# Performance work log

Hardware: AMD Instinct MI355X
Metric: run time of the kernel (lower is better)

## Reference

```python
import jax, jax.numpy as jnp
import numpy as np

N_ENT = 200000  # entities per graph (sr and tg)
E = 4_000_000   # triples per graph
R_SR, R_TG, D = 1000, 1200, 128


def _cosine_sim_nbyn(a, b):
    a = a * jax.lax.rsqrt(jnp.sum(a * a, -1, keepdims=True) + 1e-8)
    b = b * jax.lax.rsqrt(jnp.sum(b * b, -1, keepdims=True) + 1e-8)
    return a @ b.T


def _relation_weighting(a, b):
    # pad to square, cosine similarity, max-pool rows/cols (MuGNN RelationWeighting)
    ra, rb = a.shape[0], b.shape[0]
    n = max(ra, rb)
    a_p = jnp.pad(a, ((0, n - ra), (0, 0)))
    b_p = jnp.pad(b, ((0, n - rb), (0, 0)))
    sim = _cosine_sim_nbyn(a_p, b_p)  # [n, n]
    return jnp.max(sim, axis=1)[:ra], jnp.max(sim, axis=0)[:rb]


def _normalize_adj(rows, cols, vals, n):
    # symmetric normalization D^-1/2 A D^-1/2 on COO values
    deg = jax.ops.segment_sum(vals, rows, num_segments=n)
    d_is = jnp.where(deg > 0, jax.lax.rsqrt(jnp.maximum(deg, 1e-12)), 0.0)
    return vals * d_is[rows] * d_is[cols]


def _adjacency_side(head, tail, conf, imp, pca, n):
    # g_func_template: elementwise product of the three aligned sparse matrices
    vals = conf * imp * pca
    # + unit (identity) matrix, then normalize; coords = [edges ; diagonal]
    diag = jnp.arange(n)
    rows = jnp.concatenate([head, diag])
    cols = jnp.concatenate([tail, diag])
    allv = jnp.concatenate([vals, jnp.ones((n,), vals.dtype)])
    return _normalize_adj(rows, cols, allv, n)  # [E+n] COO values


def setup_inputs() -> dict:
    key = jax.random.key(0)
    ks = jax.random.split(key, 14)
    return {
        "rel_emb_sr": jax.random.normal(ks[0], (R_SR, D), jnp.float32),
        "rel_emb_tg": jax.random.normal(ks[1], (R_TG, D), jnp.float32),
        "conf_sr": jax.random.uniform(ks[2], (E,), jnp.float32),
        "imp_sr": jax.random.uniform(ks[3], (E,), jnp.float32),
        "pca_sr": jax.random.uniform(ks[4], (E,), jnp.float32),
        "conf_tg": jax.random.uniform(ks[5], (E,), jnp.float32),
        "imp_tg": jax.random.uniform(ks[6], (E,), jnp.float32),
        "pca_tg": jax.random.uniform(ks[7], (E,), jnp.float32),
        "head_sr": jax.random.randint(ks[8], (E,), 0, N_ENT),
        "tail_sr": jax.random.randint(ks[9], (E,), 0, N_ENT),
        "relation_sr": jax.random.randint(ks[10], (E,), 0, R_SR),
        "head_tg": jax.random.randint(ks[11], (E,), 0, N_ENT),
        "tail_tg": jax.random.randint(ks[12], (E,), 0, N_ENT),
        "relation_tg": jax.random.randint(ks[13], (E,), 0, R_TG),
    }


def reference(rel_emb_sr, rel_emb_tg, conf_sr, imp_sr, pca_sr,
              conf_tg, imp_tg, pca_tg,
              head_sr, tail_sr, relation_sr, head_tg, tail_tg, relation_tg):
    # relation weighting (computed in the original forward; g_func_template
    # discards the gathered relation attention, so relation_sr/tg do not
    # affect the adjacency values)
    rw_sr, rw_tg = _relation_weighting(rel_emb_sr, rel_emb_tg)
    adj_sr = _adjacency_side(head_sr, tail_sr, conf_sr, imp_sr, pca_sr, N_ENT)
    adj_tg = _adjacency_side(head_tg, tail_tg, conf_tg, imp_tg, pca_tg, N_ENT)
    # adjacency returned as normalized COO values on constant coords
    return adj_sr, adj_tg, rw_sr, rw_tg
```

## Files before the change

kernel.cpp:

```cpp
#include <hip/hip_runtime.h>
#include <stdint.h>

#define N_ENT 200000
#define NEDGE 4000000
#define RSR 1000
#define RTG 1200
#define DIM 128

#define NBUCK 196
#define BUCKSZ 1024
#define CAP 22272
#define CHUNK 4096
#define NE4 (NEDGE / 4)
#define NBLK 977
#define PER (NEDGE + N_ENT)
#define PER4 (PER / 4)
#define ATILES 16
#define BTILES 19
#define NRW 2240

typedef float f32x4 __attribute__((ext_vector_type(4)));
typedef int   i32x4 __attribute__((ext_vector_type(4)));


__global__ void prep_kernel(const float* __restrict__ emb_sr, const float* __restrict__ emb_tg,
                            float* __restrict__ an, float* __restrict__ bn,
                            unsigned* __restrict__ gcount) {
    int blk = blockIdx.x, t = threadIdx.x;
    const float* src; float* dst; int row;
    if (blk < RSR) { src = emb_sr; dst = an; row = blk; }
    else           { src = emb_tg; dst = bn; row = blk - RSR; }
    float x = src[row * DIM + t];
    __shared__ float sh[DIM];
    sh[t] = x * x;
    __syncthreads();
    for (int off = 64; off > 0; off >>= 1) {
        if (t < off) sh[t] += sh[t + off];
        __syncthreads();
    }
    dst[row * DIM + t] = x * rsqrtf(sh[0] + 1e-8f);
    if (blk == 0)
        for (int i = t; i < 2 * NBUCK; i += DIM) gcount[i] = 0;
}


__global__ __launch_bounds__(256) void passA_kernel(
        const float* __restrict__ conf_sr, const float* __restrict__ imp_sr,
        const float* __restrict__ pca_sr,
        const float* __restrict__ conf_tg, const float* __restrict__ imp_tg,
        const float* __restrict__ pca_tg,
        const int* __restrict__ head_sr, const int* __restrict__ head_tg,
        float* __restrict__ out_sr, float* __restrict__ out_tg,
        unsigned* __restrict__ gcount, unsigned* __restrict__ regions) {
    __shared__ unsigned cnt[NBUCK];
    __shared__ unsigned offs[NBUCK];
    __shared__ unsigned gdst[NBUCK];
    __shared__ unsigned ssum[256];
    __shared__ unsigned wtot[4];
    __shared__ unsigned stage[CHUNK];

    const int t = threadIdx.x;
    const int side = (int)blockIdx.x >= NBLK;
    const int blk = side ? blockIdx.x - NBLK : blockIdx.x;
    const f32x4* conf4 = (const f32x4*)(side ? conf_tg : conf_sr);
    const f32x4* imp4  = (const f32x4*)(side ? imp_tg  : imp_sr);
    const f32x4* pca4  = (const f32x4*)(side ? pca_tg  : pca_sr);
    const i32x4* head4 = (const i32x4*)(side ? head_tg : head_sr);
    f32x4*       o4    = (f32x4*)(side ? out_tg : out_sr);

    for (int i = t; i < NBUCK; i += 256) cnt[i] = 0;
    __syncthreads();

    int bkt[16];
    unsigned rec[16], rnk[16];
#pragma unroll
    for (int i = 0; i < 4; i++) {
        int q = blk * 1024 + t + i * 256;
        if (q < NE4) {
            f32x4 cf = __builtin_nontemporal_load(conf4 + q);
            f32x4 im = __builtin_nontemporal_load(imp4 + q);
            f32x4 pc = __builtin_nontemporal_load(pca4 + q);
            i32x4 hh = __builtin_nontemporal_load(head4 + q);
            f32x4 v = cf * im * pc;
            __builtin_nontemporal_store(v, o4 + q);
            const int hs[4] = {hh.x, hh.y, hh.z, hh.w};
            const float vs[4] = {v.x, v.y, v.z, v.w};
#pragma unroll
            for (int j = 0; j < 4; j++) {
                int h = hs[j];
                int bb = h >> 10;
                unsigned qv = (unsigned)(vs[j] * 16384.f + 0.5f);
                if (qv > 16383u) qv = 16383u;
                bkt[i * 4 + j] = bb;
                rec[i * 4 + j] = ((unsigned)h << 14) | qv;
                rnk[i * 4 + j] = atomicAdd(&cnt[bb], 1u);
            }
        } else {
#pragma unroll
            for (int j = 0; j < 4; j++) bkt[i * 4 + j] = -1;
        }
    }
    __syncthreads();

    {
        int lane = t & 63, w = t >> 6;
        unsigned s = (t < NBUCK) ? cnt[t] : 0u;
#pragma unroll
        for (int d = 1; d < 64; d <<= 1) {
            unsigned u = __shfl_up(s, d);
            if (lane >= d) s += u;
        }
        if (lane == 63) wtot[w] = s;
        ssum[t] = s;
    }
    __syncthreads();
    unsigned wb0 = wtot[0];
    unsigned wb1 = wb0 + wtot[1];
    unsigned wb2 = wb1 + wtot[2];
    unsigned total = wb2 + wtot[3];
    if (t < NBUCK) {
        int w = t >> 6;
        unsigned add = (w == 0) ? 0u : (w == 1) ? wb0 : (w == 2) ? wb1 : wb2;
        unsigned ex = ssum[t] + add - cnt[t];
        offs[t] = ex;
        unsigned gb = atomicAdd(&gcount[side * NBUCK + t], cnt[t]);
        gdst[t] = (unsigned)(side * NBUCK + t) * CAP + gb - ex;
    }
    __syncthreads();

#pragma unroll
    for (int i = 0; i < 16; i++)
        if (bkt[i] >= 0) stage[offs[bkt[i]] + rnk[i]] = rec[i];
    __syncthreads();

    for (int i = t; i < (int)total; i += 256) {
        unsigned r = stage[i];
        unsigned b = r >> 24;
        unsigned d = gdst[b] + i;
        if (d < (unsigned)(side * NBUCK + b + 1) * CAP)
            __builtin_nontemporal_store(r, regions + d);
    }
}


__global__ __launch_bounds__(256) void passB_kernel(const unsigned* __restrict__ regions,
                                                    const unsigned* __restrict__ gcount,
                                                    float* __restrict__ dis) {
    __shared__ float bins[BUCKSZ / 2];
    int t = threadIdx.x;
    int g = blockIdx.x;
    int sb = g >> 1;
    unsigned half = g & 1;
    for (int i = t; i < BUCKSZ / 2; i += 256) bins[i] = 0.f;
    __syncthreads();
    unsigned n = gcount[sb];
    if (n > CAP) n = CAP;
    const unsigned* rp = regions + (size_t)sb * CAP;
    for (unsigned i = t; i < n; i += 256) {
        unsigned r = __builtin_nontemporal_load(rp + i);
        unsigned bin = (r >> 14) & (BUCKSZ - 1);
        if ((bin >> 9) == half)
            atomicAdd(&bins[bin & 511u], (float)(r & 16383u) * (1.f / 16384.f));
    }
    __syncthreads();
    int side = sb >= NBUCK;
    int b = side ? sb - NBUCK : sb;
    int base = b * BUCKSZ + (int)half * 512;
    float* dout = dis + (size_t)side * N_ENT;
    for (int i = t; i < 512; i += 256) {
        int e = base + i;
        if (e < N_ENT) dout[e] = rsqrtf(1.0f + bins[i]);
    }
}


__global__ void deg_init_kernel(float* __restrict__ dis) {
    int i = blockIdx.x * 256 + threadIdx.x;
    if (i < (2 * N_ENT) / 4)
        ((float4*)dis)[i] = make_float4(1.f, 1.f, 1.f, 1.f);
}

__global__ void scatter_atomic_kernel(
        const float* __restrict__ conf_sr, const float* __restrict__ imp_sr,
        const float* __restrict__ pca_sr,
        const float* __restrict__ conf_tg, const float* __restrict__ imp_tg,
        const float* __restrict__ pca_tg,
        const int* __restrict__ head_sr, const int* __restrict__ head_tg,
        float* __restrict__ out_sr, float* __restrict__ out_tg,
        float* __restrict__ deg) {
    int e = blockIdx.x * blockDim.x + threadIdx.x;
    if (e < NEDGE) {
        float v = conf_sr[e] * imp_sr[e] * pca_sr[e];
        out_sr[e] = v;
        unsafeAtomicAdd(&deg[head_sr[e]], v);
    } else if (e < 2 * NEDGE) {
        int i = e - NEDGE;
        float v = conf_tg[i] * imp_tg[i] * pca_tg[i];
        out_tg[i] = v;
        unsafeAtomicAdd(&deg[N_ENT + head_tg[i]], v);
    }
}

__global__ void rsqrt_kernel(float* __restrict__ dis) {
    int i = blockIdx.x * blockDim.x + threadIdx.x;
    if (i < 2 * N_ENT) dis[i] = rsqrtf(dis[i]);
}


__global__ __launch_bounds__(256) void finalize_kernel(
        const int* __restrict__ head_sr, const int* __restrict__ tail_sr,
        const int* __restrict__ head_tg, const int* __restrict__ tail_tg,
        const float* __restrict__ dis, float* __restrict__ out,
        const float* __restrict__ rowpart, const float* __restrict__ colpart,
        float* __restrict__ rw_sr, float* __restrict__ rw_tg) {
    int idx = blockIdx.x * blockDim.x + threadIdx.x;
    if (idx >= 2 * PER4) {
        int rid = idx - 2 * PER4;
        if (rid < 1024) {
            if (rid < RSR) {
                float m = -1e30f;
                for (int b = 0; b < BTILES; b++) m = fmaxf(m, rowpart[b * 1024 + rid]);
                rw_sr[rid] = m;
            }
        } else if (rid < NRW) {
            int j = rid - 1024;
            if (j < RTG) {
                float m = -1e30f;
                for (int a = 0; a < ATILES; a++) m = fmaxf(m, colpart[a * 1216 + j]);
                rw_tg[j] = fmaxf(m, 0.0f);
            }
        }
        return;
    }
    int side = idx >= PER4 ? 1 : 0;
    int q = side ? idx - PER4 : idx;
    const float* dg = dis + (size_t)side * N_ENT;
    f32x4* o = (f32x4*)(out + (size_t)side * PER);
    if (q < NE4) {
        const i32x4* hd = (const i32x4*)(side ? head_tg : head_sr);
        const i32x4* tl = (const i32x4*)(side ? tail_tg : tail_sr);
        i32x4 hh = __builtin_nontemporal_load(hd + q);
        i32x4 tt = __builtin_nontemporal_load(tl + q);
        f32x4 v = __builtin_nontemporal_load(o + q);
        v.x *= dg[hh.x] * dg[tt.x];
        v.y *= dg[hh.y] * dg[tt.y];
        v.z *= dg[hh.z] * dg[tt.z];
        v.w *= dg[hh.w] * dg[tt.w];
        __builtin_nontemporal_store(v, o + q);
    } else {
        f32x4 d = ((const f32x4*)dg)[q - NE4];
        f32x4 r = d * d;
        __builtin_nontemporal_store(r, o + q);
    }
}


__global__ __launch_bounds__(256) void pools_tiles_kernel(
        const float* __restrict__ an, const float* __restrict__ bn,
        float* __restrict__ rowpart, float* __restrict__ colpart) {
    __shared__ float sA[64][132];
    __shared__ float sB[64][133];
    __shared__ float rr[64][17];
    __shared__ float cc[64][17];
    int t = threadIdx.x;
    int atile = blockIdx.x % ATILES;
    int btile = blockIdx.x / ATILES;
    for (int idx = t; idx < 64 * 32; idx += 256) {
        int row = idx >> 5, k4 = idx & 31;
        int ga = atile * 64 + row;
        float4 va = (ga < RSR) ? ((const float4*)(an + ga * DIM))[k4]
                               : make_float4(0.f, 0.f, 0.f, 0.f);
        *(float4*)&sA[row][k4 * 4] = va;
        int gb = btile * 64 + row;
        float4 vb = (gb < RTG) ? ((const float4*)(bn + gb * DIM))[k4]
                               : make_float4(0.f, 0.f, 0.f, 0.f);
        sB[row][k4 * 4 + 0] = vb.x; sB[row][k4 * 4 + 1] = vb.y;
        sB[row][k4 * 4 + 2] = vb.z; sB[row][k4 * 4 + 3] = vb.w;
    }
    __syncthreads();
    int tx = t & 15, ty = t >> 4;
    float acc[4][4] = {};
    for (int k4 = 0; k4 < 32; k4++) {
        float4 a4[4];
#pragma unroll
        for (int r = 0; r < 4; r++) a4[r] = *(const float4*)&sA[ty * 4 + r][k4 * 4];
#pragma unroll
        for (int kk = 0; kk < 4; kk++) {
            float bv[4];
#pragma unroll
            for (int c = 0; c < 4; c++) bv[c] = sB[tx * 4 + c][k4 * 4 + kk];
            float av[4];
#pragma unroll
            for (int r = 0; r < 4; r++)
                av[r] = kk == 0 ? a4[r].x : kk == 1 ? a4[r].y : kk == 2 ? a4[r].z : a4[r].w;
#pragma unroll
            for (int r = 0; r < 4; r++)
#pragma unroll
                for (int c = 0; c < 4; c++) acc[r][c] = fmaf(av[r], bv[c], acc[r][c]);
        }
    }
    float rm[4] = {-1e30f, -1e30f, -1e30f, -1e30f};
    float cm[4] = {-1e30f, -1e30f, -1e30f, -1e30f};
#pragma unroll
    for (int r = 0; r < 4; r++)
#pragma unroll
        for (int c = 0; c < 4; c++) {
            bool jok = (btile * 64 + tx * 4 + c) < RTG;
            rm[r] = fmaxf(rm[r], jok ? acc[r][c] : -1e30f);
            cm[c] = fmaxf(cm[c], acc[r][c]);
        }
#pragma unroll
    for (int r = 0; r < 4; r++) rr[ty * 4 + r][tx] = rm[r];
#pragma unroll
    for (int c = 0; c < 4; c++) cc[tx * 4 + c][ty] = cm[c];
    __syncthreads();
    if (t < 64) {
        float m = rr[t][0];
        for (int x = 1; x < 16; x++) m = fmaxf(m, rr[t][x]);
        rowpart[btile * 1024 + atile * 64 + t] = m;
        float m2 = cc[t][0];
        for (int x = 1; x < 16; x++) m2 = fmaxf(m2, cc[t][x]);
        colpart[atile * 1216 + btile * 64 + t] = m2;
    }
}


extern "C" void kernel_launch(void* const* d_in, const int* in_sizes, int n_in,
                              void* d_out, int out_size, void* d_ws, size_t ws_size,
                              hipStream_t stream) {
    const float* rel_emb_sr = (const float*)d_in[0];
    const float* rel_emb_tg = (const float*)d_in[1];
    const float* conf_sr = (const float*)d_in[2];
    const float* imp_sr  = (const float*)d_in[3];
    const float* pca_sr  = (const float*)d_in[4];
    const float* conf_tg = (const float*)d_in[5];
    const float* imp_tg  = (const float*)d_in[6];
    const float* pca_tg  = (const float*)d_in[7];
    const int* head_sr = (const int*)d_in[8];
    const int* tail_sr = (const int*)d_in[9];
    const int* head_tg = (const int*)d_in[11];
    const int* tail_tg = (const int*)d_in[12];

    float* out = (float*)d_out;
    float* out_sr = out;
    float* out_tg = out + PER;
    float* rw_sr  = out + 2 * (size_t)PER;
    float* rw_tg  = rw_sr + RSR;

    float* ws = (float*)d_ws;
    float* an  = ws;
    float* bn  = an + RSR * DIM;
    float* dis = bn + RTG * DIM;
    unsigned* gcount  = (unsigned*)(dis + 2 * N_ENT);
    unsigned* regions = gcount + 512;
    float* rowpart = (float*)(regions + (size_t)2 * NBUCK * CAP);
    float* colpart = rowpart + BTILES * 1024;

    size_t need = ((size_t)(RSR * DIM + RTG * DIM + 2 * N_ENT + 512) +
                   (size_t)2 * NBUCK * CAP + BTILES * 1024 + ATILES * 1216) * 4;
    bool bucketed = ws_size >= need;

    hipLaunchKernelGGL(prep_kernel, dim3(RSR + RTG), dim3(DIM), 0, stream,
                       rel_emb_sr, rel_emb_tg, an, bn, gcount);

    if (bucketed) {
        hipLaunchKernelGGL(passA_kernel, dim3(2 * NBLK), dim3(256), 0, stream,
                           conf_sr, imp_sr, pca_sr, conf_tg, imp_tg, pca_tg,
                           head_sr, head_tg, out_sr, out_tg, gcount, regions);
        hipLaunchKernelGGL(passB_kernel, dim3(4 * NBUCK), dim3(256), 0, stream,
                           regions, gcount, dis);
    } else {
        hipLaunchKernelGGL(deg_init_kernel, dim3((2 * N_ENT / 4 + 255) / 256), dim3(256),
                           0, stream, dis);
        hipLaunchKernelGGL(scatter_atomic_kernel, dim3((2 * NEDGE + 255) / 256), dim3(256),
                           0, stream,
                           conf_sr, imp_sr, pca_sr, conf_tg, imp_tg, pca_tg,
                           head_sr, head_tg, out_sr, out_tg, dis);
        hipLaunchKernelGGL(rsqrt_kernel, dim3((2 * N_ENT + 255) / 256), dim3(256), 0, stream,
                           dis);
    }

    hipLaunchKernelGGL(pools_tiles_kernel, dim3(ATILES * BTILES), dim3(256), 0, stream,
                       an, bn, rowpart, colpart);

    hipLaunchKernelGGL(finalize_kernel, dim3((2 * PER4 + NRW + 255) / 256), dim3(256),
                       0, stream,
                       head_sr, tail_sr, head_tg, tail_tg, dis, out,
                       rowpart, colpart, rw_sr, rw_tg);
}
```

Before: 391.4 us.

## Double passA block size and drop nontemporal hints on reused streams

Pass A now runs 512-thread blocks, each covering twice as many edges with a larger shared staging buffer. This halves the block count and the per-block global bucket atomics, and gives longer contiguous runs per bucket when regions are written. Nontemporal loads and stores are replaced with ordinary ones for head indices, the product output, the bucket regions and the final scaling pass, so data reused by later kernels can stay in cache. The cost is higher shared memory per block, which may lower occupancy, plus possible cache pollution.

```diff
diff --git a/kernel.cpp b/kernel.cpp
--- a/kernel.cpp
+++ b/kernel.cpp
@@ -10,9 +10,10 @@
 #define NBUCK 196
 #define BUCKSZ 1024
 #define CAP 22272
-#define CHUNK 4096
+#define CHUNK 8192
+#define NTA 512
 #define NE4 (NEDGE / 4)
-#define NBLK 977
+#define NBLK 489
 #define PER (NEDGE + N_ENT)
 #define PER4 (PER / 4)
 #define ATILES 16
@@ -44,7 +45,7 @@
 }
 
 
-__global__ __launch_bounds__(256) void passA_kernel(
+__global__ __launch_bounds__(NTA) void passA_kernel(
         const float* __restrict__ conf_sr, const float* __restrict__ imp_sr,
         const float* __restrict__ pca_sr,
         const float* __restrict__ conf_tg, const float* __restrict__ imp_tg,
@@ -68,21 +69,21 @@
     const i32x4* head4 = (const i32x4*)(side ? head_tg : head_sr);
     f32x4*       o4    = (f32x4*)(side ? out_tg : out_sr);
 
-    for (int i = t; i < NBUCK; i += 256) cnt[i] = 0;
+    for (int i = t; i < NBUCK; i += NTA) cnt[i] = 0;
     __syncthreads();
 
     int bkt[16];
     unsigned rec[16], rnk[16];
 #pragma unroll
     for (int i = 0; i < 4; i++) {
-        int q = blk * 1024 + t + i * 256;
+        int q = blk * 2048 + t + i * NTA;
         if (q < NE4) {
             f32x4 cf = __builtin_nontemporal_load(conf4 + q);
             f32x4 im = __builtin_nontemporal_load(imp4 + q);
             f32x4 pc = __builtin_nontemporal_load(pca4 + q);
-            i32x4 hh = __builtin_nontemporal_load(head4 + q);
+            i32x4 hh = head4[q];
             f32x4 v = cf * im * pc;
-            __builtin_nontemporal_store(v, o4 + q);
+            o4[q] = v;
             const int hs[4] = {hh.x, hh.y, hh.z, hh.w};
             const float vs[4] = {v.x, v.y, v.z, v.w};
 #pragma unroll
@@ -102,7 +103,7 @@
     }
     __syncthreads();
 
-    {
+    if (t < 256) {
         int lane = t & 63, w = t >> 6;
         unsigned s = (t < NBUCK) ? cnt[t] : 0u;
 #pragma unroll
@@ -133,12 +134,11 @@
         if (bkt[i] >= 0) stage[offs[bkt[i]] + rnk[i]] = rec[i];
     __syncthreads();
 
-    for (int i = t; i < (int)total; i += 256) {
+    for (int i = t; i < (int)total; i += NTA) {
         unsigned r = stage[i];
         unsigned b = r >> 24;
         unsigned d = gdst[b] + i;
-        if (d < (unsigned)(side * NBUCK + b + 1) * CAP)
-            __builtin_nontemporal_store(r, regions + d);
+        if (d < (unsigned)(side * NBUCK + b + 1) * CAP) regions[d] = r;
     }
 }
 
@@ -157,7 +157,7 @@
     if (n > CAP) n = CAP;
     const unsigned* rp = regions + (size_t)sb * CAP;
     for (unsigned i = t; i < n; i += 256) {
-        unsigned r = __builtin_nontemporal_load(rp + i);
+        unsigned r = rp[i];
         unsigned bin = (r >> 14) & (BUCKSZ - 1);
         if ((bin >> 9) == half)
             atomicAdd(&bins[bin & 511u], (float)(r & 16383u) * (1.f / 16384.f));
@@ -239,18 +239,17 @@
     if (q < NE4) {
         const i32x4* hd = (const i32x4*)(side ? head_tg : head_sr);
         const i32x4* tl = (const i32x4*)(side ? tail_tg : tail_sr);
-        i32x4 hh = __builtin_nontemporal_load(hd + q);
-        i32x4 tt = __builtin_nontemporal_load(tl + q);
-        f32x4 v = __builtin_nontemporal_load(o + q);
+        i32x4 hh = hd[q];
+        i32x4 tt = tl[q];
+        f32x4 v = o[q];
         v.x *= dg[hh.x] * dg[tt.x];
         v.y *= dg[hh.y] * dg[tt.y];
         v.z *= dg[hh.z] * dg[tt.z];
         v.w *= dg[hh.w] * dg[tt.w];
-        __builtin_nontemporal_store(v, o + q);
+        o[q] = v;
     } else {
         f32x4 d = ((const f32x4*)dg)[q - NE4];
-        f32x4 r = d * d;
-        __builtin_nontemporal_store(r, o + q);
+        o[q] = d * d;
     }
 }
 
@@ -364,7 +363,7 @@
                        rel_emb_sr, rel_emb_tg, an, bn, gcount);
 
     if (bucketed) {
-        hipLaunchKernelGGL(passA_kernel, dim3(2 * NBLK), dim3(256), 0, stream,
+        hipLaunchKernelGGL(passA_kernel, dim3(2 * NBLK), dim3(NTA), 0, stream,
                            conf_sr, imp_sr, pca_sr, conf_tg, imp_tg, pca_tg,
                            head_sr, head_tg, out_sr, out_tg, gcount, regions);
         hipLaunchKernelGGL(passB_kernel, dim3(4 * NBUCK), dim3(256), 0, stream,
```

Result: faster. 358.0 us (-8.5%).
